# Optimization experiments

Hardware: AMD Instinct MI355X
Metric: run time of the kernel (lower is better)

The kernel has to match this reference:

```python
import jax, jax.numpy as jnp
import numpy as np
from jax import lax

DIM = 64
B, H, W = 4, 256, 256


def setup_inputs() -> dict:
    key = jax.random.key(0)
    ks = jax.random.split(key, 6)
    d = DIM
    x = jax.random.normal(ks[0], (B, d, H, W), dtype=jnp.float32)
    w_hidden = jax.random.normal(ks[1], (6 * d, d), dtype=jnp.float32) * 0.05      # 1x1 conv dim->6*dim
    w_dw = jax.random.normal(ks[2], (6 * d, 1, 3, 3), dtype=jnp.float32) * 0.05    # depthwise 3x3
    norm_w = jnp.ones((2 * d,), dtype=jnp.float32)
    norm_b = jnp.zeros((2 * d,), dtype=jnp.float32)
    w_out = jax.random.normal(ks[3], (d, 2 * d), dtype=jnp.float32) * 0.05         # 1x1 conv 2*dim->dim
    return {"x": x, "w_hidden": w_hidden, "w_dw": w_dw,
            "norm_w": norm_w, "norm_b": norm_b, "w_out": w_out, "patch_size": 8}


def reference(x, w_hidden, w_dw, norm_w, norm_b, w_out, patch_size):
    p = patch_size
    b, c, h, w = x.shape
    # 1x1 conv: dim -> 6*dim
    hidden = jnp.einsum('oc,bchw->bohw', w_hidden, x)
    # depthwise 3x3 conv, padding=1
    hidden = lax.conv_general_dilated(
        hidden, w_dw, window_strides=(1, 1), padding='SAME',
        dimension_numbers=('NCHW', 'OIHW', 'NCHW'),
        feature_group_count=w_dw.shape[0])
    q, k, v = jnp.split(hidden, 3, axis=1)  # each [b, 2c, h, w]

    c2 = 2 * c
    def to_patch(t):  # b c (h p1) (w p2) -> b c h w p1 p2
        return t.reshape(b, c2, h // p, p, w // p, p).transpose(0, 1, 2, 4, 3, 5)

    q_fft = jnp.fft.rfft2(to_patch(q).astype(jnp.float32))
    k_fft = jnp.fft.rfft2(to_patch(k).astype(jnp.float32))
    out = jnp.fft.irfft2(q_fft * k_fft, s=(p, p))  # circular conv per patch
    # b c h w p1 p2 -> b c (h p1) (w p2)
    out = out.transpose(0, 1, 2, 4, 3, 5).reshape(b, c2, h, w)

    # WithBias LayerNorm over channel dim (to_3d normalizes last dim = channels)
    mu = out.mean(axis=1, keepdims=True)
    var = out.var(axis=1, keepdims=True)
    out_norm = (out - mu) / jnp.sqrt(var + 1e-5)
    out_norm = out_norm * norm_w[None, :, None, None] + norm_b[None, :, None, None]

    gated = v * out_norm
    # 1x1 conv: 2*dim -> dim
    return jnp.einsum('oc,bchw->bohw', w_out, gated)
```

## Files before the change

kernel.cpp:

```cpp
#include <hip/hip_runtime.h>


typedef _Float16 f16x8 __attribute__((ext_vector_type(8)));
typedef _Float16 f16x4 __attribute__((ext_vector_type(4)));
typedef _Float16 f16x2 __attribute__((ext_vector_type(2)));
typedef __fp16   h16x2 __attribute__((ext_vector_type(2)));
typedef float    f32x4 __attribute__((ext_vector_type(4)));

#define XS_OFF    0
#define HS_OFF    14336
#define QCC_OFF   27136
#define TMP_OFF   44544
#define MU_OFF    53248
#define RSTD_OFF  53504
#define LNW_OFF   53760
#define LNB_OFF   54016
#define LDS_BYTES 54272

__global__ __launch_bounds__(512, 4) void lfsa_fused(
    const float* __restrict__ x,
    const float* __restrict__ wh,
    const float* __restrict__ wdw,
    const float* __restrict__ nw,
    const float* __restrict__ nb,
    const float* __restrict__ wo,
    float* __restrict__ out)
{
    extern __shared__ char lds[];
    _Float16* xs    = (_Float16*)(lds + XS_OFF);
    _Float16* hs    = (_Float16*)(lds + HS_OFF);
    _Float16* qcc16 = (_Float16*)(lds + QCC_OFF);
    _Float16* tmp16 = (_Float16*)(lds + TMP_OFF);
    _Float16* gs16  = (_Float16*)(lds + TMP_OFF);
    float*    mu_s  = (float*)(lds + MU_OFF);
    float*    rstd_s= (float*)(lds + RSTD_OFF);
    _Float16* lnw16 = (_Float16*)(lds + LNW_OFF);
    _Float16* lnb16 = (_Float16*)(lds + LNB_OFF);

    const int tid = threadIdx.x;
    const int px = blockIdx.x, py = blockIdx.y, bz = blockIdx.z;
    const int lane = tid & 63;
    const int wv   = tid >> 6;
    const int m16  = lane & 15;
    const int quad = lane >> 4;

    {
        const int pix  = tid & 127;
        const int gg   = tid >> 7;
        const int prow = pix / 10;
        const int pcol = pix - prow * 10;
        const int yy = py * 8 + prow - 1;
        const int xx = px * 8 + pcol - 1;
        const bool inimg = (pix < 100) && ((unsigned)yy < 256u) && ((unsigned)xx < 256u);
        if (pix < 112) {
            const float* xp = inimg
                ? (x + (size_t)((bz * 64 + gg * 16) * 65536 + yy * 256 + xx)) : x;
            f16x8 lo, hi;
            #pragma unroll
            for (int i = 0; i < 8; ++i) {
                lo[i] = (_Float16)(inimg ? xp[(size_t)i * 65536] : 0.0f);
                hi[i] = (_Float16)(inimg ? xp[(size_t)(i + 8) * 65536] : 0.0f);
            }
            const int s = pix & 7;
            _Float16* xrow = xs + pix * 64;
            *(f16x8*)(xrow + (((2 * gg)     ^ s) * 8)) = lo;
            *(f16x8*)(xrow + (((2 * gg + 1) ^ s) * 8)) = hi;
        }
        if (tid < 128) { lnw16[tid] = (_Float16)nw[tid]; lnb16[tid] = (_Float16)nb[tid]; }
    }

    const int dwo = tid >> 3;
    const int blk = tid & 7;
    const int by2 = (blk >> 1) * 2;
    const int bx4 = (blk & 1) * 4;
    const int ci  = tid & 7;

    const int ot = wv >> 1;
    const float* wha = wh + (size_t)(ot * 16 + m16) * 64 + quad * 8;
    float4 wr0 = *(const float4*)(wha);
    float4 wr1 = *(const float4*)(wha + 4);
    float4 wr2 = *(const float4*)(wha + 32);
    float4 wr3 = *(const float4*)(wha + 36);

    f32x4 pacc2[2] = {{0.f,0.f,0.f,0.f},{0.f,0.f,0.f,0.f}};

    __syncthreads();

    #pragma unroll 1
    for (int kc = 0; kc < 6; ++kc) {
        const f16x8 a0 = {(_Float16)wr0.x,(_Float16)wr0.y,(_Float16)wr0.z,(_Float16)wr0.w,
                          (_Float16)wr1.x,(_Float16)wr1.y,(_Float16)wr1.z,(_Float16)wr1.w};
        const f16x8 a1 = {(_Float16)wr2.x,(_Float16)wr2.y,(_Float16)wr2.z,(_Float16)wr2.w,
                          (_Float16)wr3.x,(_Float16)wr3.y,(_Float16)wr3.z,(_Float16)wr3.w};
        if (kc < 5) {
            const float* nx = wha + (size_t)(kc + 1) * 4096;
            wr0 = *(const float4*)(nx);
            wr1 = *(const float4*)(nx + 4);
            wr2 = *(const float4*)(nx + 32);
            wr3 = *(const float4*)(nx + 36);
        }
        float w9c[9];
        #pragma unroll
        for (int t = 0; t < 9; ++t) w9c[t] = wdw[(kc * 64 + dwo) * 9 + t];

        {
            const int np  = (wv & 1) ? 3 : 4;
            const int pt0 = (wv & 1) * 4;
            for (int pp = 0; pp < np; ++pp) {
                const int pt = pt0 + pp;
                const int pixg = pt * 16 + m16;
                const _Float16* xrow = xs + pixg * 64;
                const int c0 = ((quad ^ (pixg & 7)) * 8);
                const f16x8 b0 = *(const f16x8*)(xrow + c0);
                const f16x8 b1 = *(const f16x8*)(xrow + (c0 ^ 32));
                f32x4 d = {0.f,0.f,0.f,0.f};
                d = __builtin_amdgcn_mfma_f32_16x16x32_f16(a0, b0, d, 0, 0, 0);
                d = __builtin_amdgcn_mfma_f32_16x16x32_f16(a1, b1, d, 0, 0, 0);
                if (pixg < 100) {
                    const int oloc = ot * 16 + quad * 4;
                    #pragma unroll
                    for (int r = 0; r < 4; ++r)
                        hs[100 * (oloc + r) + pixg] = (_Float16)d[r];
                }
            }
        }
        __syncthreads();

        if (kc < 4) {
            const _Float16* hrow = hs + 100 * dwo;
            float in[4][6];
            #pragma unroll
            for (int r = 0; r < 4; ++r) {
                const _Float16* rp = hrow + (by2 + r) * 10 + bx4;
                const f16x2 p0 = *(const f16x2*)rp;
                const f16x2 p1 = *(const f16x2*)(rp + 2);
                const f16x2 p2 = *(const f16x2*)(rp + 4);
                in[r][0] = (float)p0[0]; in[r][1] = (float)p0[1];
                in[r][2] = (float)p1[0]; in[r][3] = (float)p1[1];
                in[r][4] = (float)p2[0]; in[r][5] = (float)p2[1];
            }
            #pragma unroll
            for (int r = 0; r < 2; ++r) {
                float rv[4];
                #pragma unroll
                for (int c = 0; c < 4; ++c) {
                    float s = 0.0f;
                    #pragma unroll
                    for (int dy = 0; dy < 3; ++dy)
                        #pragma unroll
                        for (int dx = 0; dx < 3; ++dx)
                            s = fmaf(w9c[dy * 3 + dx], in[r + dy][c + dx], s);
                    rv[c] = s;
                }
                const int off = (by2 + r) * 8 + bx4;
                _Float16* dst = (kc < 2) ? (qcc16 + 68 * (kc * 64 + dwo))
                                         : (tmp16 + 68 * dwo);
                *(f16x4*)(dst + off) = f16x4{(_Float16)rv[0], (_Float16)rv[1],
                                             (_Float16)rv[2], (_Float16)rv[3]};
            }
        } else {
            const _Float16* hrow = hs + 100 * dwo;
            const int chg = (kc - 4) * 64 + dwo;
            const float lw = (float)lnw16[chg], lb = (float)lnb16[chg];
            const _Float16* ccrow = qcc16 + 68 * chg;
            #pragma unroll
            for (int half = 0; half < 2; ++half) {
                float cA[6], cB[6], cC[6];
                #pragma unroll
                for (int rr = 0; rr < 6; ++rr) {
                    const int row = half * 4 + rr;
                    cA[rr] = (float)hrow[row * 10 + blk];
                    cB[rr] = (float)hrow[row * 10 + blk + 1];
                    cC[rr] = (float)hrow[row * 10 + blk + 2];
                }
                #pragma unroll
                for (int r = 0; r < 4; ++r) {
                    float s = 0.0f;
                    #pragma unroll
                    for (int dy = 0; dy < 3; ++dy) {
                        s = fmaf(w9c[dy * 3 + 0], cA[r + dy], s);
                        s = fmaf(w9c[dy * 3 + 1], cB[r + dy], s);
                        s = fmaf(w9c[dy * 3 + 2], cC[r + dy], s);
                    }
                    const int p = (half * 4 + r) * 8 + blk;
                    const float nrm = ((float)ccrow[p] - mu_s[p]) * rstd_s[p] * lw + lb;
                    gs16[p * 68 + dwo] = (_Float16)(s * nrm);
                }
            }
        }

        if (kc == 2 || kc == 3) {
            const int ch = (kc - 2) * 64 + dwo;
            _Float16* qrow = qcc16 + 68 * ch;
            const _Float16* krow = tmp16 + 68 * dwo;
            float acc[8];
            #pragma unroll
            for (int j = 0; j < 8; ++j) acc[j] = 0.0f;
            #pragma unroll
            for (int a = 0; a < 8; ++a) {
                const f16x8 qv = *(const f16x8*)(qrow + 8 * a);
                h16x2 q2[4];
                #pragma unroll
                for (int t = 0; t < 4; ++t) {
                    q2[t][0] = (__fp16)qv[2 * t];
                    q2[t][1] = (__fp16)qv[2 * t + 1];
                }
                const int r = (ci - a) & 7;
                const f16x8 kr = *(const f16x8*)(krow + 8 * r);
                h16x2 rp[8];
                #pragma unroll
                for (int i = 0; i < 8; ++i)
                    rp[i] = h16x2{(__fp16)kr[i], (__fp16)kr[(i + 7) & 7]};
                #pragma unroll
                for (int j = 0; j < 8; ++j)
                    #pragma unroll
                    for (int t = 0; t < 4; ++t)
                        acc[j] = __builtin_amdgcn_fdot2(q2[t], rp[(j - 2 * t) & 7],
                                                        acc[j], false);
            }
            *(f16x4*)(qrow + 8 * ci)     = f16x4{(_Float16)acc[0], (_Float16)acc[1],
                                                 (_Float16)acc[2], (_Float16)acc[3]};
            *(f16x4*)(qrow + 8 * ci + 4) = f16x4{(_Float16)acc[4], (_Float16)acc[5],
                                                 (_Float16)acc[6], (_Float16)acc[7]};
        }
        __syncthreads();

        if (kc == 3) {
            const int p = 8 * wv + (lane & 7);
            const int g = lane >> 3;
            float s = 0.0f, s2v = 0.0f;
            #pragma unroll
            for (int i = 0; i < 16; ++i) {
                const float v = (float)qcc16[68 * (g + 8 * i) + p];
                s += v; s2v = fmaf(v, v, s2v);
            }
            #pragma unroll
            for (int m = 8; m < 64; m <<= 1) {
                s   += __shfl_xor(s, m, 64);
                s2v += __shfl_xor(s2v, m, 64);
            }
            if (lane < 8) {
                const float mu = s * (1.0f / 128.0f);
                mu_s[p]   = mu;
                rstd_s[p] = rsqrtf(s2v * (1.0f / 128.0f) - mu * mu + 1e-5f);
            }
        }

        if (kc >= 4) {
            const int cb = (kc - 4) * 64;
            const float* wop = wo + (size_t)(ot * 16 + m16) * 128 + cb + quad * 8;
            const float4 u0 = *(const float4*)(wop);
            const float4 u1 = *(const float4*)(wop + 4);
            const float4 u2 = *(const float4*)(wop + 32);
            const float4 u3 = *(const float4*)(wop + 36);
            const f16x8 pa0 = {(_Float16)u0.x,(_Float16)u0.y,(_Float16)u0.z,(_Float16)u0.w,
                               (_Float16)u1.x,(_Float16)u1.y,(_Float16)u1.z,(_Float16)u1.w};
            const f16x8 pa1 = {(_Float16)u2.x,(_Float16)u2.y,(_Float16)u2.z,(_Float16)u2.w,
                               (_Float16)u3.x,(_Float16)u3.y,(_Float16)u3.z,(_Float16)u3.w};
            #pragma unroll
            for (int tt = 0; tt < 2; ++tt) {
                const int pt = (wv & 1) * 2 + tt;
                const _Float16* bp = gs16 + (pt * 16 + m16) * 68 + quad * 8;
                const f16x8 b0 = *(const f16x8*)bp;
                const f16x8 b1 = *(const f16x8*)(bp + 32);
                pacc2[tt] = __builtin_amdgcn_mfma_f32_16x16x32_f16(pa0, b0, pacc2[tt], 0, 0, 0);
                pacc2[tt] = __builtin_amdgcn_mfma_f32_16x16x32_f16(pa1, b1, pacc2[tt], 0, 0, 0);
            }
        }
    }

    {
        #pragma unroll
        for (int tt = 0; tt < 2; ++tt) {
            const int pixg = ((wv & 1) * 2 + tt) * 16 + m16;
            const int r = pixg >> 3, c = pixg & 7;
            float* op = out + (size_t)(bz * 64 + ot * 16 + quad * 4) * 65536
                            + (py * 8 + r) * 256 + px * 8 + c;
            #pragma unroll
            for (int reg = 0; reg < 4; ++reg)
                op[(size_t)reg * 65536] = pacc2[tt][reg];
        }
    }
}

extern "C" void kernel_launch(void* const* d_in, const int* in_sizes, int n_in,
                              void* d_out, int out_size, void* d_ws, size_t ws_size,
                              hipStream_t stream) {
    const float* x   = (const float*)d_in[0];
    const float* wh  = (const float*)d_in[1];
    const float* wdw = (const float*)d_in[2];
    const float* nw  = (const float*)d_in[3];
    const float* nb  = (const float*)d_in[4];
    const float* wo  = (const float*)d_in[5];
    float* outp = (float*)d_out;

    (void)hipFuncSetAttribute((const void*)lfsa_fused,
                              hipFuncAttributeMaxDynamicSharedMemorySize, LDS_BYTES);
    dim3 grid(32, 32, 4);
    lfsa_fused<<<grid, 512, LDS_BYTES, stream>>>(x, wh, wdw, nw, nb, wo, outp);
}
```

Measured before the change: 393.5 us.

## Fuse LayerNorm statistics into circular-conv epilogue and vectorize gated depthwise stage

Channel sums and sums of squares are now accumulated from the fp32 circular-convolution results in registers via cross-lane shuffles, then reduced across waves through a small LDS scratch, instead of re-reading all 128 fp16 channels from LDS afterwards. This also computes the statistics from unrounded fp32 values. The kc>=4 depthwise+gating path switches to a 2x4 pixel tile per thread with vectorized LDS loads of inputs, mu and rstd. The cost is an extra barrier, more live registers and extra shuffles in the kc 2/3 loop.

```diff
diff --git a/kernel.cpp b/kernel.cpp
--- a/kernel.cpp
+++ b/kernel.cpp
@@ -32,6 +32,8 @@
     _Float16* qcc16 = (_Float16*)(lds + QCC_OFF);
     _Float16* tmp16 = (_Float16*)(lds + TMP_OFF);
     _Float16* gs16  = (_Float16*)(lds + TMP_OFF);
+    float*    scrS  = (float*)(lds + TMP_OFF);
+    float*    scrQ  = scrS + 512;
     float*    mu_s  = (float*)(lds + MU_OFF);
     float*    rstd_s= (float*)(lds + RSTD_OFF);
     _Float16* lnw16 = (_Float16*)(lds + LNW_OFF);
@@ -83,6 +85,7 @@
     float4 wr3 = *(const float4*)(wha + 36);
 
     f32x4 pacc2[2] = {{0.f,0.f,0.f,0.f},{0.f,0.f,0.f,0.f}};
+    float sS2[8], sQ2[8];
 
     __syncthreads();
 
@@ -163,28 +166,33 @@
             const int chg = (kc - 4) * 64 + dwo;
             const float lw = (float)lnw16[chg], lb = (float)lnb16[chg];
             const _Float16* ccrow = qcc16 + 68 * chg;
-            #pragma unroll
-            for (int half = 0; half < 2; ++half) {
-                float cA[6], cB[6], cC[6];
-                #pragma unroll
-                for (int rr = 0; rr < 6; ++rr) {
-                    const int row = half * 4 + rr;
-                    cA[rr] = (float)hrow[row * 10 + blk];
-                    cB[rr] = (float)hrow[row * 10 + blk + 1];
-                    cC[rr] = (float)hrow[row * 10 + blk + 2];
-                }
-                #pragma unroll
-                for (int r = 0; r < 4; ++r) {
+            float in[4][6];
+            #pragma unroll
+            for (int r = 0; r < 4; ++r) {
+                const _Float16* rp = hrow + (by2 + r) * 10 + bx4;
+                const f16x2 p0 = *(const f16x2*)rp;
+                const f16x2 p1 = *(const f16x2*)(rp + 2);
+                const f16x2 p2 = *(const f16x2*)(rp + 4);
+                in[r][0] = (float)p0[0]; in[r][1] = (float)p0[1];
+                in[r][2] = (float)p1[0]; in[r][3] = (float)p1[1];
+                in[r][4] = (float)p2[0]; in[r][5] = (float)p2[1];
+            }
+            #pragma unroll
+            for (int r = 0; r < 2; ++r) {
+                const int prow = by2 + r;
+                const f16x4 cc4 = *(const f16x4*)(ccrow + prow * 8 + bx4);
+                const f32x4 mu4 = *(const f32x4*)(mu_s + prow * 8 + bx4);
+                const f32x4 rs4 = *(const f32x4*)(rstd_s + prow * 8 + bx4);
+                #pragma unroll
+                for (int c = 0; c < 4; ++c) {
                     float s = 0.0f;
                     #pragma unroll
-                    for (int dy = 0; dy < 3; ++dy) {
-                        s = fmaf(w9c[dy * 3 + 0], cA[r + dy], s);
-                        s = fmaf(w9c[dy * 3 + 1], cB[r + dy], s);
-                        s = fmaf(w9c[dy * 3 + 2], cC[r + dy], s);
-                    }
-                    const int p = (half * 4 + r) * 8 + blk;
-                    const float nrm = ((float)ccrow[p] - mu_s[p]) * rstd_s[p] * lw + lb;
-                    gs16[p * 68 + dwo] = (_Float16)(s * nrm);
+                    for (int dy = 0; dy < 3; ++dy)
+                        #pragma unroll
+                        for (int dx = 0; dx < 3; ++dx)
+                            s = fmaf(w9c[dy * 3 + dx], in[r + dy][c + dx], s);
+                    const float nrm = ((float)cc4[c] - mu4[c]) * rs4[c] * lw + lb;
+                    gs16[(prow * 8 + bx4 + c) * 68 + dwo] = (_Float16)(s * nrm);
                 }
             }
         }
@@ -218,6 +226,19 @@
                         acc[j] = __builtin_amdgcn_fdot2(q2[t], rp[(j - 2 * t) & 7],
                                                         acc[j], false);
             }
+            #pragma unroll
+            for (int j = 0; j < 8; ++j) {
+                float sS = acc[j];
+                float sQ = acc[j] * acc[j];
+                sS += __shfl_xor(sS, 8, 64);
+                sQ += __shfl_xor(sQ, 8, 64);
+                sS += __shfl_xor(sS, 16, 64);
+                sQ += __shfl_xor(sQ, 16, 64);
+                sS += __shfl_xor(sS, 32, 64);
+                sQ += __shfl_xor(sQ, 32, 64);
+                if (kc == 2) { sS2[j] = sS; sQ2[j] = sQ; }
+                else         { sS2[j] += sS; sQ2[j] += sQ; }
+            }
             *(f16x4*)(qrow + 8 * ci)     = f16x4{(_Float16)acc[0], (_Float16)acc[1],
                                                  (_Float16)acc[2], (_Float16)acc[3]};
             *(f16x4*)(qrow + 8 * ci + 4) = f16x4{(_Float16)acc[4], (_Float16)acc[5],
@@ -226,23 +247,25 @@
         __syncthreads();
 
         if (kc == 3) {
-            const int p = 8 * wv + (lane & 7);
-            const int g = lane >> 3;
-            float s = 0.0f, s2v = 0.0f;
-            #pragma unroll
-            for (int i = 0; i < 16; ++i) {
-                const float v = (float)qcc16[68 * (g + 8 * i) + p];
-                s += v; s2v = fmaf(v, v, s2v);
-            }
-            #pragma unroll
-            for (int m = 8; m < 64; m <<= 1) {
-                s   += __shfl_xor(s, m, 64);
-                s2v += __shfl_xor(s2v, m, 64);
-            }
             if (lane < 8) {
-                const float mu = s * (1.0f / 128.0f);
-                mu_s[p]   = mu;
-                rstd_s[p] = rsqrtf(s2v * (1.0f / 128.0f) - mu * mu + 1e-5f);
+                const int base = wv * 64 + ci * 8;
+                *(f32x4*)(scrS + base)     = f32x4{sS2[0], sS2[1], sS2[2], sS2[3]};
+                *(f32x4*)(scrS + base + 4) = f32x4{sS2[4], sS2[5], sS2[6], sS2[7]};
+                *(f32x4*)(scrQ + base)     = f32x4{sQ2[0], sQ2[1], sQ2[2], sQ2[3]};
+                *(f32x4*)(scrQ + base + 4) = f32x4{sQ2[4], sQ2[5], sQ2[6], sQ2[7]};
+            }
+            __syncthreads();
+            if (tid < 64) {
+                float S = 0.0f, Q = 0.0f;
+                #pragma unroll
+                for (int w = 0; w < 8; ++w) {
+                    S += scrS[w * 64 + tid];
+                    Q += scrQ[w * 64 + tid];
+                }
+                const float sm = S * 0.0078125f;
+                const float sq = Q * 0.0078125f;
+                mu_s[tid]   = sm;
+                rstd_s[tid] = rsqrtf(sq - sm * sm + 1e-5f);
             }
         }
 
```

Measured after the change: 410.7 us. +4.4%, slower.
